# Optimization experiments

Measured on AMD Instinct MI355X. Metric: run time of the kernel, lower is better.

Reference implementation:

```python
import jax, jax.numpy as jnp
import numpy as np

IN_DIM = 256
K = 64
NB = 64  # num_blocks
N = NB * K
BATCH = 4096
DT = 0.05
TAU_EPS = 1e-6


def setup_inputs() -> dict:
    key = jax.random.key(0)
    ks = jax.random.split(key, 10)
    def xavier(k_, shape, fan_in, fan_out):
        lim = np.sqrt(6.0 / (fan_in + fan_out))
        return jax.random.uniform(k_, shape, jnp.float32, -lim, lim)
    return {
        "y": jax.random.normal(ks[0], (BATCH, N), jnp.float32),
        "u_t": jax.random.normal(ks[1], (BATCH, IN_DIM), jnp.float32),
        "tau_raw": jnp.zeros((N,), jnp.float32),
        "W_in_w": xavier(ks[2], (K, IN_DIM), IN_DIM, K),
        "W_in_b": jnp.zeros((K,), jnp.float32),
        "W_fwd_w": xavier(ks[3], (NB - 1, K, K), K, K),
        "W_fwd_b": jnp.zeros((NB - 1, K), jnp.float32),
        "W_rec_w": xavier(ks[4], (NB, K, K), K, K),
        "W_rec_b": jnp.zeros((NB, K), jnp.float32),
        "E_l": xavier(ks[5], (NB, K, K), K, K),
        "E_l_r": xavier(ks[6], (NB, K, K), K, K),
    }


def reference(y, u_t, tau_raw, W_in_w, W_in_b, W_fwd_w, W_fwd_b, W_rec_w, W_rec_b, E_l, E_l_r):
    yb = y.reshape(-1, NB, K)  # [batch, B, k]
    tau = jax.nn.softplus(tau_raw).reshape(NB, K) + TAU_EPS  # [B, k]
    # input drive for block 0 (torch Linear: x @ W^T + b)
    net0 = jnp.tanh(u_t @ W_in_w.T + W_in_b)  # [batch, k]
    # forward coupling for blocks 1..B-1, batched over blocks
    prev = yb[:, :-1, :]  # [batch, B-1, k]
    net_fwd = jnp.tanh(jnp.einsum('bji,joi->bjo', prev, W_fwd_w) + W_fwd_b)
    net_out = jnp.concatenate([net0[:, None, :], net_fwd], axis=1)  # [batch, B, k]
    # recurrent coupling, all blocks
    net_rec = jnp.tanh(jnp.einsum('bji,joi->bjo', yb, W_rec_w) + W_rec_b)
    decay = 1.0 / tau + jnp.abs(net_out) + jnp.abs(net_rec)  # [batch, B, k]
    drive = jnp.einsum('joi,bji->bjo', E_l, net_out) + jnp.einsum('joi,bji->bjo', E_l_r, net_rec)
    y_new = (yb + DT * drive) / (1.0 + DT * decay)
    return y_new.reshape(-1, N)
```

## Files before the change

### kernel.cpp

```cpp
#include <hip/hip_runtime.h>


#define IN_DIM 256
#define K 64
#define NB 64
#define BATCH 4096
#define NTOT (NB * K)
#define DTC 0.05f
#define TAU_EPS 1e-6f
#define LDSTR 72

typedef __bf16 bf16;
typedef bf16 bf16x8 __attribute__((ext_vector_type(8)));
typedef bf16 bf16x4 __attribute__((ext_vector_type(4)));
typedef float f32x4 __attribute__((ext_vector_type(4)));

__device__ __forceinline__ float fast_tanh(float x) {
    float e = __expf(2.0f * x);
    return 1.0f - 2.0f * __builtin_amdgcn_rcpf(e + 1.0f);
}

__device__ __forceinline__ void stage64(bf16* __restrict__ dst,
                                        const float* __restrict__ src,
                                        int gstride, int tid) {
#pragma unroll
    for (int it = 0; it < 4; ++it) {
        int idx = it * 256 + tid;
        int r = idx >> 4;
        int c4 = idx & 15;
        float4 v = *(const float4*)(src + r * gstride + (c4 << 2));
        bf16x4 p = { (bf16)v.x, (bf16)v.y, (bf16)v.z, (bf16)v.w };
        *(bf16x4*)(dst + r * LDSTR + (c4 << 2)) = p;
    }
}

__device__ __forceinline__ void load_afrag(const float* __restrict__ rowp,
                                           bf16x8& f0, bf16x8& f1) {
    float4 a0 = *(const float4*)(rowp);
    float4 a1 = *(const float4*)(rowp + 4);
    float4 a2 = *(const float4*)(rowp + 32);
    float4 a3 = *(const float4*)(rowp + 36);
    f0 = (bf16x8){ (bf16)a0.x, (bf16)a0.y, (bf16)a0.z, (bf16)a0.w,
                   (bf16)a1.x, (bf16)a1.y, (bf16)a1.z, (bf16)a1.w };
    f1 = (bf16x8){ (bf16)a2.x, (bf16)a2.y, (bf16)a2.z, (bf16)a2.w,
                   (bf16)a3.x, (bf16)a3.y, (bf16)a3.z, (bf16)a3.w };
}

__global__ __launch_bounds__(256, 4)
void ltcn_kernel(const float* __restrict__ y, const float* __restrict__ u_t,
                 const float* __restrict__ tau_raw,
                 const float* __restrict__ W_in_w, const float* __restrict__ W_in_b,
                 const float* __restrict__ W_fwd_w, const float* __restrict__ W_fwd_b,
                 const float* __restrict__ W_rec_w, const float* __restrict__ W_rec_b,
                 const float* __restrict__ E_l, const float* __restrict__ E_l_r,
                 float* __restrict__ out) {
    __shared__ bf16 sWf [64 * LDSTR];
    __shared__ bf16 sWr [64 * LDSTR];
    __shared__ bf16 sEl [64 * LDSTR];
    __shared__ bf16 sElr[64 * LDSTR];
    __shared__ float sInvTau[64], sBf[64], sBr[64];

    const int tid  = threadIdx.x;
    const int j    = blockIdx.y;
    const int b0   = blockIdx.x * 64;
    const int wave = tid >> 6;
    const int lane = tid & 63;
    const int quad = lane >> 4;
    const int l16  = lane & 15;
    const int am   = wave * 16 + l16;

    stage64(sWr,  W_rec_w + (size_t)j * K * K, K, tid);
    stage64(sEl,  E_l     + (size_t)j * K * K, K, tid);
    stage64(sElr, E_l_r   + (size_t)j * K * K, K, tid);

    bf16x8 yc0, yc1;
    load_afrag(y + (size_t)(b0 + am) * NTOT + j * K + quad * 8, yc0, yc1);

    bf16x8 yp0, yp1;
    if (j != 0) {
        stage64(sWf, W_fwd_w + (size_t)(j - 1) * K * K, K, tid);
        load_afrag(y + (size_t)(b0 + am) * NTOT + (j - 1) * K + quad * 8, yp0, yp1);
    } else {
        stage64(sWf, W_in_w, IN_DIM, tid);
        load_afrag(u_t + (size_t)(b0 + am) * IN_DIM + quad * 8, yp0, yp1);
    }
    if (tid < 64) {
        float x = tau_raw[j * K + tid];
        float sp = (x > 15.0f) ? x : log1pf(__expf(x));
        sInvTau[tid] = 1.0f / (sp + TAU_EPS);
        sBf[tid] = (j == 0) ? W_in_b[tid] : W_fwd_b[(j - 1) * K + tid];
        sBr[tid] = W_rec_b[j * K + tid];
    }
    __syncthreads();

    f32x4 accF[4] = {}, accR[4] = {};
    const int boff = quad * 8;
    if (j != 0) {
#pragma unroll
        for (int ct = 0; ct < 4; ++ct) {
            const bf16* br = sWr + (ct * 16 + l16) * LDSTR + boff;
            const bf16* bw = sWf + (ct * 16 + l16) * LDSTR + boff;
            accR[ct] = __builtin_amdgcn_mfma_f32_16x16x32_bf16(yc0, *(const bf16x8*)br,        accR[ct], 0, 0, 0);
            accR[ct] = __builtin_amdgcn_mfma_f32_16x16x32_bf16(yc1, *(const bf16x8*)(br + 32), accR[ct], 0, 0, 0);
            accF[ct] = __builtin_amdgcn_mfma_f32_16x16x32_bf16(yp0, *(const bf16x8*)bw,        accF[ct], 0, 0, 0);
            accF[ct] = __builtin_amdgcn_mfma_f32_16x16x32_bf16(yp1, *(const bf16x8*)(bw + 32), accF[ct], 0, 0, 0);
        }
    } else {
#pragma unroll
        for (int ct = 0; ct < 4; ++ct) {
            const bf16* br = sWr + (ct * 16 + l16) * LDSTR + boff;
            accR[ct] = __builtin_amdgcn_mfma_f32_16x16x32_bf16(yc0, *(const bf16x8*)br,        accR[ct], 0, 0, 0);
            accR[ct] = __builtin_amdgcn_mfma_f32_16x16x32_bf16(yc1, *(const bf16x8*)(br + 32), accR[ct], 0, 0, 0);
        }
        for (int kc = 0; kc < 4; ++kc) {
#pragma unroll
            for (int ct = 0; ct < 4; ++ct) {
                const bf16* bw = sWf + (ct * 16 + l16) * LDSTR + boff;
                accF[ct] = __builtin_amdgcn_mfma_f32_16x16x32_bf16(yp0, *(const bf16x8*)bw,        accF[ct], 0, 0, 0);
                accF[ct] = __builtin_amdgcn_mfma_f32_16x16x32_bf16(yp1, *(const bf16x8*)(bw + 32), accF[ct], 0, 0, 0);
            }
            if (kc < 3) {
                load_afrag(u_t + (size_t)(b0 + am) * IN_DIM + (kc + 1) * 64 + quad * 8, yp0, yp1);
                __syncthreads();
                stage64(sWf, W_in_w + (kc + 1) * 64, IN_DIM, tid);
                __syncthreads();
            }
        }
    }

    float absum[4][4];
#pragma unroll
    for (int ct = 0; ct < 4; ++ct) {
        float bfv = sBf[ct * 16 + l16];
        float brv = sBr[ct * 16 + l16];
#pragma unroll
        for (int r = 0; r < 4; ++r) {
            float no = fast_tanh(accF[ct][r] + bfv);
            float nr = fast_tanh(accR[ct][r] + brv);
            accF[ct][r] = no;
            accR[ct][r] = nr;
            absum[ct][r] = fabsf(no) + fabsf(nr);
        }
    }
    __syncthreads();

#pragma unroll
    for (int ct = 0; ct < 4; ++ct) {
#pragma unroll
        for (int r = 0; r < 4; ++r) {
            int m = wave * 16 + quad * 4 + r;
            int n = ct * 16 + l16;
            sWf[m * LDSTR + n] = (bf16)accF[ct][r];
            sWr[m * LDSTR + n] = (bf16)accR[ct][r];
        }
    }
    __syncthreads();

    float ye[4][4];
    const float* yep = y + (size_t)(b0 + wave * 16 + quad * 4) * NTOT + (size_t)j * K + l16;
#pragma unroll
    for (int ct = 0; ct < 4; ++ct)
#pragma unroll
        for (int r = 0; r < 4; ++r)
            ye[ct][r] = yep[(size_t)r * NTOT + ct * 16];

    const bf16* aOp = sWf + am * LDSTR + quad * 8;
    const bf16* aRp = sWr + am * LDSTR + quad * 8;
    bf16x8 aO0 = *(const bf16x8*)aOp,        aO1 = *(const bf16x8*)(aOp + 32);
    bf16x8 aR0 = *(const bf16x8*)aRp,        aR1 = *(const bf16x8*)(aRp + 32);

    f32x4 accD[4] = {};
#pragma unroll
    for (int ct = 0; ct < 4; ++ct) {
        const bf16* bo = sEl  + (ct * 16 + l16) * LDSTR + quad * 8;
        const bf16* br = sElr + (ct * 16 + l16) * LDSTR + quad * 8;
        accD[ct] = __builtin_amdgcn_mfma_f32_16x16x32_bf16(aO0, *(const bf16x8*)bo,        accD[ct], 0, 0, 0);
        accD[ct] = __builtin_amdgcn_mfma_f32_16x16x32_bf16(aO1, *(const bf16x8*)(bo + 32), accD[ct], 0, 0, 0);
        accD[ct] = __builtin_amdgcn_mfma_f32_16x16x32_bf16(aR0, *(const bf16x8*)br,        accD[ct], 0, 0, 0);
        accD[ct] = __builtin_amdgcn_mfma_f32_16x16x32_bf16(aR1, *(const bf16x8*)(br + 32), accD[ct], 0, 0, 0);
    }

    float it4[4];
#pragma unroll
    for (int ct = 0; ct < 4; ++ct) it4[ct] = sInvTau[ct * 16 + l16];

#pragma unroll
    for (int ct = 0; ct < 4; ++ct) {
#pragma unroll
        for (int r = 0; r < 4; ++r) {
            size_t gi = (size_t)(b0 + wave * 16 + quad * 4 + r) * NTOT + j * K + ct * 16 + l16;
            float decay = it4[ct] + absum[ct][r];
            out[gi] = (ye[ct][r] + DTC * accD[ct][r]) * __builtin_amdgcn_rcpf(1.0f + DTC * decay);
        }
    }
}

extern "C" void kernel_launch(void* const* d_in, const int* in_sizes, int n_in,
                              void* d_out, int out_size, void* d_ws, size_t ws_size,
                              hipStream_t stream) {
    const float* y       = (const float*)d_in[0];
    const float* u_t     = (const float*)d_in[1];
    const float* tau_raw = (const float*)d_in[2];
    const float* W_in_w  = (const float*)d_in[3];
    const float* W_in_b  = (const float*)d_in[4];
    const float* W_fwd_w = (const float*)d_in[5];
    const float* W_fwd_b = (const float*)d_in[6];
    const float* W_rec_w = (const float*)d_in[7];
    const float* W_rec_b = (const float*)d_in[8];
    const float* E_l     = (const float*)d_in[9];
    const float* E_l_r   = (const float*)d_in[10];
    float* out = (float*)d_out;

    dim3 grid(BATCH / 64, NB);
    hipLaunchKernelGGL(ltcn_kernel, grid, dim3(256), 0, stream,
                       y, u_t, tau_raw, W_in_w, W_in_b, W_fwd_w, W_fwd_b,
                       W_rec_w, W_rec_b, E_l, E_l_r, out);
}
```

Before: 163.4 us.

## Pre-permute weights to bf16 fragment layout and read them directly from global

A new pre-pass kernel converts all weight matrices to bf16 and writes them to workspace in the exact MFMA B-fragment order. The main kernel then loads B fragments straight from global/L2 instead of staging fp32 weights into LDS with conversion and barriers. This removes per-block weight staging traffic and most __syncthreads, and lets occupancy rise from 4 to 6 blocks per CU. It also drops the LDS tables for biases and tau in favour of per-thread registers. The cost is an extra kernel launch plus more scattered global loads in the MFMA loop; the tanh-output LDS round trip now relies on each wave reading only its own rows.

```diff
diff --git a/kernel.cpp b/kernel.cpp
--- a/kernel.cpp
+++ b/kernel.cpp
@@ -5,14 +5,20 @@
 #define K 64
 #define NB 64
 #define BATCH 4096
-#define NTOT (NB * K)
+#define NTOT 4096
 #define DTC 0.05f
 #define TAU_EPS 1e-6f
-#define LDSTR 72
+#define NSTR 72
+
+#define WS_WREC 0
+#define WS_EL   (64 * 4096)
+#define WS_ELR  (128 * 4096)
+#define WS_WFWD (192 * 4096)
+#define WS_WIN  (255 * 4096)
+#define WS_BLOCKS 259
 
 typedef __bf16 bf16;
 typedef bf16 bf16x8 __attribute__((ext_vector_type(8)));
-typedef bf16 bf16x4 __attribute__((ext_vector_type(4)));
 typedef float f32x4 __attribute__((ext_vector_type(4)));
 
 __device__ __forceinline__ float fast_tanh(float x) {
@@ -20,18 +26,9 @@
     return 1.0f - 2.0f * __builtin_amdgcn_rcpf(e + 1.0f);
 }
 
-__device__ __forceinline__ void stage64(bf16* __restrict__ dst,
-                                        const float* __restrict__ src,
-                                        int gstride, int tid) {
-#pragma unroll
-    for (int it = 0; it < 4; ++it) {
-        int idx = it * 256 + tid;
-        int r = idx >> 4;
-        int c4 = idx & 15;
-        float4 v = *(const float4*)(src + r * gstride + (c4 << 2));
-        bf16x4 p = { (bf16)v.x, (bf16)v.y, (bf16)v.z, (bf16)v.w };
-        *(bf16x4*)(dst + r * LDSTR + (c4 << 2)) = p;
-    }
+__device__ __forceinline__ bf16x8 bfrag(const bf16* __restrict__ base,
+                                        int kh, int ct, int lofs) {
+    return *(const bf16x8*)(base + ((((kh * 4 + ct) << 6) + lofs) << 3));
 }
 
 __device__ __forceinline__ void load_afrag(const float* __restrict__ rowp,
@@ -46,19 +43,41 @@
                    (bf16)a3.x, (bf16)a3.y, (bf16)a3.z, (bf16)a3.w };
 }
 
-__global__ __launch_bounds__(256, 4)
-void ltcn_kernel(const float* __restrict__ y, const float* __restrict__ u_t,
-                 const float* __restrict__ tau_raw,
-                 const float* __restrict__ W_in_w, const float* __restrict__ W_in_b,
-                 const float* __restrict__ W_fwd_w, const float* __restrict__ W_fwd_b,
-                 const float* __restrict__ W_rec_w, const float* __restrict__ W_rec_b,
-                 const float* __restrict__ E_l, const float* __restrict__ E_l_r,
-                 float* __restrict__ out) {
-    __shared__ bf16 sWf [64 * LDSTR];
-    __shared__ bf16 sWr [64 * LDSTR];
-    __shared__ bf16 sEl [64 * LDSTR];
-    __shared__ bf16 sElr[64 * LDSTR];
-    __shared__ float sInvTau[64], sBf[64], sBr[64];
+__global__ __launch_bounds__(256)
+void perm_weights(const float* __restrict__ W_in_w, const float* __restrict__ W_fwd_w,
+                  const float* __restrict__ W_rec_w, const float* __restrict__ E_l,
+                  const float* __restrict__ E_l_r, bf16* __restrict__ wsb) {
+    const int g = blockIdx.x;
+    const float* src;
+    int stride;
+    if (g < 64)       { src = W_rec_w + (size_t)g * 4096;         stride = 64;  }
+    else if (g < 128) { src = E_l     + (size_t)(g - 64) * 4096;  stride = 64;  }
+    else if (g < 192) { src = E_l_r   + (size_t)(g - 128) * 4096; stride = 64;  }
+    else if (g < 255) { src = W_fwd_w + (size_t)(g - 192) * 4096; stride = 64;  }
+    else              { src = W_in_w + (g - 255) * 64;            stride = 256; }
+    bf16* dst = wsb + (size_t)g * 4096;
+    const int tid = threadIdx.x;
+#pragma unroll
+    for (int h = 0; h < 2; ++h) {
+        int c = tid * 2 + h;
+        int kh = c >> 8, ct = (c >> 6) & 3, l16 = (c >> 2) & 15, quad = c & 3;
+        const float* s = src + (ct * 16 + l16) * stride + kh * 32 + quad * 8;
+        float4 a = *(const float4*)s;
+        float4 b = *(const float4*)(s + 4);
+        bf16x8 p = { (bf16)a.x, (bf16)a.y, (bf16)a.z, (bf16)a.w,
+                     (bf16)b.x, (bf16)b.y, (bf16)b.z, (bf16)b.w };
+        *(bf16x8*)(dst + (size_t)c * 8) = p;
+    }
+}
+
+__global__ __launch_bounds__(256, 6)
+void ltcn_main(const float* __restrict__ y, const float* __restrict__ u_t,
+               const float* __restrict__ tau_raw,
+               const float* __restrict__ W_in_b, const float* __restrict__ W_fwd_b,
+               const float* __restrict__ W_rec_b,
+               const bf16* __restrict__ wsb, float* __restrict__ out) {
+    __shared__ bf16 sNO[64 * NSTR];
+    __shared__ bf16 sNR[64 * NSTR];
 
     const int tid  = threadIdx.x;
     const int j    = blockIdx.y;
@@ -68,62 +87,48 @@
     const int quad = lane >> 4;
     const int l16  = lane & 15;
     const int am   = wave * 16 + l16;
+    const int lofs = l16 * 4 + quad;
 
-    stage64(sWr,  W_rec_w + (size_t)j * K * K, K, tid);
-    stage64(sEl,  E_l     + (size_t)j * K * K, K, tid);
-    stage64(sElr, E_l_r   + (size_t)j * K * K, K, tid);
-
-    bf16x8 yc0, yc1;
-    load_afrag(y + (size_t)(b0 + am) * NTOT + j * K + quad * 8, yc0, yc1);
-
-    bf16x8 yp0, yp1;
-    if (j != 0) {
-        stage64(sWf, W_fwd_w + (size_t)(j - 1) * K * K, K, tid);
-        load_afrag(y + (size_t)(b0 + am) * NTOT + (j - 1) * K + quad * 8, yp0, yp1);
-    } else {
-        stage64(sWf, W_in_w, IN_DIM, tid);
-        load_afrag(u_t + (size_t)(b0 + am) * IN_DIM + quad * 8, yp0, yp1);
+    float bfv[4], brv[4], itv[4];
+#pragma unroll
+    for (int ct = 0; ct < 4; ++ct) {
+        int n = ct * 16 + l16;
+        brv[ct] = W_rec_b[j * K + n];
+        bfv[ct] = j ? W_fwd_b[(j - 1) * K + n] : W_in_b[n];
+        float x = tau_raw[j * K + n];
+        float sp = (x > 15.0f) ? x : log1pf(__expf(x));
+        itv[ct] = 1.0f / (sp + TAU_EPS);
     }
-    if (tid < 64) {
-        float x = tau_raw[j * K + tid];
-        float sp = (x > 15.0f) ? x : log1pf(__expf(x));
-        sInvTau[tid] = 1.0f / (sp + TAU_EPS);
-        sBf[tid] = (j == 0) ? W_in_b[tid] : W_fwd_b[(j - 1) * K + tid];
-        sBr[tid] = W_rec_b[j * K + tid];
-    }
-    __syncthreads();
 
     f32x4 accF[4] = {}, accR[4] = {};
-    const int boff = quad * 8;
-    if (j != 0) {
+    {
+        bf16x8 yc0, yc1;
+        load_afrag(y + (size_t)(b0 + am) * NTOT + j * K + quad * 8, yc0, yc1);
+        const bf16* Wr = wsb + WS_WREC + (size_t)j * 4096;
 #pragma unroll
         for (int ct = 0; ct < 4; ++ct) {
-            const bf16* br = sWr + (ct * 16 + l16) * LDSTR + boff;
-            const bf16* bw = sWf + (ct * 16 + l16) * LDSTR + boff;
-            accR[ct] = __builtin_amdgcn_mfma_f32_16x16x32_bf16(yc0, *(const bf16x8*)br,        accR[ct], 0, 0, 0);
-            accR[ct] = __builtin_amdgcn_mfma_f32_16x16x32_bf16(yc1, *(const bf16x8*)(br + 32), accR[ct], 0, 0, 0);
-            accF[ct] = __builtin_amdgcn_mfma_f32_16x16x32_bf16(yp0, *(const bf16x8*)bw,        accF[ct], 0, 0, 0);
-            accF[ct] = __builtin_amdgcn_mfma_f32_16x16x32_bf16(yp1, *(const bf16x8*)(bw + 32), accF[ct], 0, 0, 0);
+            accR[ct] = __builtin_amdgcn_mfma_f32_16x16x32_bf16(yc0, bfrag(Wr, 0, ct, lofs), accR[ct], 0, 0, 0);
+            accR[ct] = __builtin_amdgcn_mfma_f32_16x16x32_bf16(yc1, bfrag(Wr, 1, ct, lofs), accR[ct], 0, 0, 0);
+        }
+    }
+    if (j) {
+        bf16x8 yp0, yp1;
+        load_afrag(y + (size_t)(b0 + am) * NTOT + (j - 1) * K + quad * 8, yp0, yp1);
+        const bf16* Wf = wsb + WS_WFWD + (size_t)(j - 1) * 4096;
+#pragma unroll
+        for (int ct = 0; ct < 4; ++ct) {
+            accF[ct] = __builtin_amdgcn_mfma_f32_16x16x32_bf16(yp0, bfrag(Wf, 0, ct, lofs), accF[ct], 0, 0, 0);
+            accF[ct] = __builtin_amdgcn_mfma_f32_16x16x32_bf16(yp1, bfrag(Wf, 1, ct, lofs), accF[ct], 0, 0, 0);
         }
     } else {
-#pragma unroll
-        for (int ct = 0; ct < 4; ++ct) {
-            const bf16* br = sWr + (ct * 16 + l16) * LDSTR + boff;
-            accR[ct] = __builtin_amdgcn_mfma_f32_16x16x32_bf16(yc0, *(const bf16x8*)br,        accR[ct], 0, 0, 0);
-            accR[ct] = __builtin_amdgcn_mfma_f32_16x16x32_bf16(yc1, *(const bf16x8*)(br + 32), accR[ct], 0, 0, 0);
-        }
         for (int kc = 0; kc < 4; ++kc) {
+            bf16x8 u0, u1;
+            load_afrag(u_t + (size_t)(b0 + am) * IN_DIM + kc * 64 + quad * 8, u0, u1);
+            const bf16* Wf = wsb + WS_WIN + (size_t)kc * 4096;
 #pragma unroll
             for (int ct = 0; ct < 4; ++ct) {
-                const bf16* bw = sWf + (ct * 16 + l16) * LDSTR + boff;
-                accF[ct] = __builtin_amdgcn_mfma_f32_16x16x32_bf16(yp0, *(const bf16x8*)bw,        accF[ct], 0, 0, 0);
-                accF[ct] = __builtin_amdgcn_mfma_f32_16x16x32_bf16(yp1, *(const bf16x8*)(bw + 32), accF[ct], 0, 0, 0);
-            }
-            if (kc < 3) {
-                load_afrag(u_t + (size_t)(b0 + am) * IN_DIM + (kc + 1) * 64 + quad * 8, yp0, yp1);
-                __syncthreads();
-                stage64(sWf, W_in_w + (kc + 1) * 64, IN_DIM, tid);
-                __syncthreads();
+                accF[ct] = __builtin_amdgcn_mfma_f32_16x16x32_bf16(u0, bfrag(Wf, 0, ct, lofs), accF[ct], 0, 0, 0);
+                accF[ct] = __builtin_amdgcn_mfma_f32_16x16x32_bf16(u1, bfrag(Wf, 1, ct, lofs), accF[ct], 0, 0, 0);
             }
         }
     }
@@ -131,66 +136,40 @@
     float absum[4][4];
 #pragma unroll
     for (int ct = 0; ct < 4; ++ct) {
-        float bfv = sBf[ct * 16 + l16];
-        float brv = sBr[ct * 16 + l16];
 #pragma unroll
         for (int r = 0; r < 4; ++r) {
-            float no = fast_tanh(accF[ct][r] + bfv);
-            float nr = fast_tanh(accR[ct][r] + brv);
-            accF[ct][r] = no;
-            accR[ct][r] = nr;
+            float no = fast_tanh(accF[ct][r] + bfv[ct]);
+            float nr = fast_tanh(accR[ct][r] + brv[ct]);
             absum[ct][r] = fabsf(no) + fabsf(nr);
+            int m = wave * 16 + quad * 4 + r;
+            int n = ct * 16 + l16;
+            sNO[m * NSTR + n] = (bf16)no;
+            sNR[m * NSTR + n] = (bf16)nr;
         }
     }
-    __syncthreads();
+    bf16x8 aO0 = *(const bf16x8*)(sNO + am * NSTR + quad * 8);
+    bf16x8 aO1 = *(const bf16x8*)(sNO + am * NSTR + quad * 8 + 32);
+    bf16x8 aR0 = *(const bf16x8*)(sNR + am * NSTR + quad * 8);
+    bf16x8 aR1 = *(const bf16x8*)(sNR + am * NSTR + quad * 8 + 32);
 
+    f32x4 accD[4] = {};
+    const bf16* El  = wsb + WS_EL  + (size_t)j * 4096;
+    const bf16* Elr = wsb + WS_ELR + (size_t)j * 4096;
 #pragma unroll
     for (int ct = 0; ct < 4; ++ct) {
-#pragma unroll
-        for (int r = 0; r < 4; ++r) {
-            int m = wave * 16 + quad * 4 + r;
-            int n = ct * 16 + l16;
-            sWf[m * LDSTR + n] = (bf16)accF[ct][r];
-            sWr[m * LDSTR + n] = (bf16)accR[ct][r];
-        }
+        accD[ct] = __builtin_amdgcn_mfma_f32_16x16x32_bf16(aO0, bfrag(El,  0, ct, lofs), accD[ct], 0, 0, 0);
+        accD[ct] = __builtin_amdgcn_mfma_f32_16x16x32_bf16(aO1, bfrag(El,  1, ct, lofs), accD[ct], 0, 0, 0);
+        accD[ct] = __builtin_amdgcn_mfma_f32_16x16x32_bf16(aR0, bfrag(Elr, 0, ct, lofs), accD[ct], 0, 0, 0);
+        accD[ct] = __builtin_amdgcn_mfma_f32_16x16x32_bf16(aR1, bfrag(Elr, 1, ct, lofs), accD[ct], 0, 0, 0);
     }
-    __syncthreads();
-
-    float ye[4][4];
-    const float* yep = y + (size_t)(b0 + wave * 16 + quad * 4) * NTOT + (size_t)j * K + l16;
-#pragma unroll
-    for (int ct = 0; ct < 4; ++ct)
-#pragma unroll
-        for (int r = 0; r < 4; ++r)
-            ye[ct][r] = yep[(size_t)r * NTOT + ct * 16];
-
-    const bf16* aOp = sWf + am * LDSTR + quad * 8;
-    const bf16* aRp = sWr + am * LDSTR + quad * 8;
-    bf16x8 aO0 = *(const bf16x8*)aOp,        aO1 = *(const bf16x8*)(aOp + 32);
-    bf16x8 aR0 = *(const bf16x8*)aRp,        aR1 = *(const bf16x8*)(aRp + 32);
-
-    f32x4 accD[4] = {};
-#pragma unroll
-    for (int ct = 0; ct < 4; ++ct) {
-        const bf16* bo = sEl  + (ct * 16 + l16) * LDSTR + quad * 8;
-        const bf16* br = sElr + (ct * 16 + l16) * LDSTR + quad * 8;
-        accD[ct] = __builtin_amdgcn_mfma_f32_16x16x32_bf16(aO0, *(const bf16x8*)bo,        accD[ct], 0, 0, 0);
-        accD[ct] = __builtin_amdgcn_mfma_f32_16x16x32_bf16(aO1, *(const bf16x8*)(bo + 32), accD[ct], 0, 0, 0);
-        accD[ct] = __builtin_amdgcn_mfma_f32_16x16x32_bf16(aR0, *(const bf16x8*)br,        accD[ct], 0, 0, 0);
-        accD[ct] = __builtin_amdgcn_mfma_f32_16x16x32_bf16(aR1, *(const bf16x8*)(br + 32), accD[ct], 0, 0, 0);
-    }
-
-    float it4[4];
-#pragma unroll
-    for (int ct = 0; ct < 4; ++ct) it4[ct] = sInvTau[ct * 16 + l16];
 
 #pragma unroll
     for (int ct = 0; ct < 4; ++ct) {
 #pragma unroll
         for (int r = 0; r < 4; ++r) {
             size_t gi = (size_t)(b0 + wave * 16 + quad * 4 + r) * NTOT + j * K + ct * 16 + l16;
-            float decay = it4[ct] + absum[ct][r];
-            out[gi] = (ye[ct][r] + DTC * accD[ct][r]) * __builtin_amdgcn_rcpf(1.0f + DTC * decay);
+            float decay = itv[ct] + absum[ct][r];
+            out[gi] = (y[gi] + DTC * accD[ct][r]) * __builtin_amdgcn_rcpf(1.0f + DTC * decay);
         }
     }
 }
@@ -210,9 +189,10 @@
     const float* E_l     = (const float*)d_in[9];
     const float* E_l_r   = (const float*)d_in[10];
     float* out = (float*)d_out;
+    bf16* wsb = (bf16*)d_ws;
 
-    dim3 grid(BATCH / 64, NB);
-    hipLaunchKernelGGL(ltcn_kernel, grid, dim3(256), 0, stream,
-                       y, u_t, tau_raw, W_in_w, W_in_b, W_fwd_w, W_fwd_b,
-                       W_rec_w, W_rec_b, E_l, E_l_r, out);
+    hipLaunchKernelGGL(perm_weights, dim3(WS_BLOCKS), dim3(256), 0, stream,
+                       W_in_w, W_fwd_w, W_rec_w, E_l, E_l_r, wsb);
+    hipLaunchKernelGGL(ltcn_main, dim3(BATCH / 64, NB), dim3(256), 0, stream,
+                       y, u_t, tau_raw, W_in_b, W_fwd_b, W_rec_b, wsb, out);
 }
```

Result: slower. 192.6 us (+17.9%).
